# Kernel tuning notes

Hardware: AMD Instinct MI355X
Metric: run time of the kernel (lower is better)

Reference implementation:

```python
import jax, jax.numpy as jnp
import numpy as np

N_NODES = 50000
N_EDGES = 800000
NODE_DIM = 128
EDGE_DIM = 10
IN_DIM = 2 * NODE_DIM + EDGE_DIM
BN_EPS = 1e-5


def setup_inputs() -> dict:
    key = jax.random.key(0)
    ks = jax.random.split(key, 8)
    h = jax.random.normal(ks[0], (N_NODES, NODE_DIM), dtype=jnp.float32)
    edge_index = jax.random.randint(ks[1], (2, N_EDGES), 0, N_NODES, dtype=jnp.int64)
    edge_feat = jax.random.normal(ks[2], (N_EDGES, EDGE_DIM), dtype=jnp.float32)
    scale = 1.0 / np.sqrt(IN_DIM)
    gate_w = jax.random.normal(ks[3], (IN_DIM, NODE_DIM), dtype=jnp.float32) * scale
    gate_b = jax.random.normal(ks[4], (NODE_DIM,), dtype=jnp.float32) * scale
    cand_w = jax.random.normal(ks[5], (IN_DIM, NODE_DIM), dtype=jnp.float32) * scale
    cand_b = jax.random.normal(ks[6], (NODE_DIM,), dtype=jnp.float32) * scale
    bn_gamma = jnp.ones((NODE_DIM,), dtype=jnp.float32)
    bn_beta = jnp.zeros((NODE_DIM,), dtype=jnp.float32)
    return {"h": h, "edge_index": edge_index, "edge_feat": edge_feat,
            "gate_w": gate_w, "gate_b": gate_b, "cand_w": cand_w, "cand_b": cand_b,
            "bn_gamma": bn_gamma, "bn_beta": bn_beta}


def reference(h, edge_index, edge_feat, gate_w, gate_b, cand_w, cand_b, bn_gamma, bn_beta):
    src = edge_index[0]
    dst = edge_index[1]
    # gather endpoint features and concat with edge features: [E, 2*D + De]
    z = jnp.concatenate([h[src], h[dst], edge_feat], axis=1)
    g = jax.nn.sigmoid(z @ gate_w + gate_b)   # [E, D]
    c = jax.nn.softplus(z @ cand_w + cand_b)  # [E, D]
    m = g * c
    # scatter-add messages to source nodes (matches index_add_(0, src, m))
    agg = jax.ops.segment_sum(m, src, num_segments=h.shape[0])
    # BatchNorm1d in training mode: batch mean / biased variance over nodes
    mean = jnp.mean(agg, axis=0)
    var = jnp.var(agg, axis=0)
    agg_bn = (agg - mean) * jax.lax.rsqrt(var + BN_EPS) * bn_gamma + bn_beta
    return jax.nn.softplus(h + agg_bn)
```

## Files before the change

### kernel.cpp

```cpp
#include <hip/hip_runtime.h>
#include <math.h>

#define N_NODES 50000
#define N_EDGES 800000
#define D 128
#define DE 10
#define K_TOT 266
#define TE 64
#define N_TILES (N_EDGES / TE)
#define ZSTRIDE 296
#define MSTRIDE 129
#define WP_ELEMS (9 * 16 * 64 * 8)
#define SCAN_BLOCKS 196
#define CSTRIDE 16

typedef __bf16 bf16x8 __attribute__((ext_vector_type(8)));
typedef __bf16 bf16x4 __attribute__((ext_vector_type(4)));
typedef __bf16 bf16x2 __attribute__((ext_vector_type(2)));
typedef float  f32x4  __attribute__((ext_vector_type(4)));

__device__ __forceinline__ float fast_sigmoid(float x) {
    float t = __builtin_amdgcn_exp2f(-1.44269504089f * x);
    return __builtin_amdgcn_rcpf(1.0f + t);
}
__device__ __forceinline__ float fast_softplus(float x) {
    float t = __builtin_amdgcn_exp2f(-1.44269504089f * fabsf(x));
    return fmaxf(x, 0.0f) + 0.69314718056f * __builtin_amdgcn_logf(1.0f + t);
}

__global__ __launch_bounds__(256) void prep(
    const float* __restrict__ h, const float* __restrict__ gw,
    const float* __restrict__ cw, const int* __restrict__ ei,
    __bf16* __restrict__ hb, __bf16* __restrict__ wp,
    int* __restrict__ counts)
{
    int bx = blockIdx.x, t = threadIdx.x;
    if (bx < 6250) {
        int i4 = bx * 256 + t;
        float4 v = *(const float4*)&h[(size_t)i4 * 4];
        bf16x4 o = { (__bf16)v.x, (__bf16)v.y, (__bf16)v.z, (__bf16)v.w };
        *(bf16x4*)&hb[(size_t)i4 * 4] = o;
    } else if (bx < 6538) {
        int idx = (bx - 6250) * 256 + t;
        if (idx < WP_ELEMS) {
            int j    = idx & 7;
            int lane = (idx >> 3) & 63;
            int nb   = (idx >> 9) & 15;
            int kb   = idx >> 13;
            int k    = kb * 32 + ((lane >> 4) << 3) + j;
            int col  = ((nb >> 1) << 4) + (lane & 15);
            const float* w = (nb & 1) ? cw : gw;
            float v = (k < K_TOT) ? w[k * D + col] : 0.0f;
            wp[idx] = (__bf16)v;
        }
    } else {
        int e = (bx - 6538) * 256 + t;
        atomicAdd(&counts[ei[e] * CSTRIDE], 1);
    }
}

__global__ __launch_bounds__(256) void scan_partials(
    const int* __restrict__ counts, int* __restrict__ bsum)
{
    __shared__ int ss[256];
    int t = threadIdx.x;
    int i = blockIdx.x * 256 + t;
    int c = (i < N_NODES) ? counts[i * CSTRIDE] : 0;
    ss[t] = c;
    __syncthreads();
    #pragma unroll
    for (int off = 1; off < 256; off <<= 1) {
        int v = (t >= off) ? ss[t - off] : 0;
        __syncthreads();
        ss[t] += v;
        __syncthreads();
    }
    if (t == 255) bsum[blockIdx.x] = ss[255];
}

__global__ __launch_bounds__(256) void scan_final(
    int* __restrict__ counts, const int* __restrict__ bsum)
{
    __shared__ int sb[256];
    __shared__ int ss[256];
    int t = threadIdx.x;
    sb[t] = (t < SCAN_BLOCKS) ? bsum[t] : 0;
    int i = blockIdx.x * 256 + t;
    int c = (i < N_NODES) ? counts[i * CSTRIDE] : 0;
    ss[t] = c;
    __syncthreads();
    #pragma unroll
    for (int off = 1; off < 256; off <<= 1) {
        int v  = (t >= off) ? ss[t - off] : 0;
        int vb = (t >= off) ? sb[t - off] : 0;
        __syncthreads();
        ss[t] += v;
        sb[t] += vb;
        __syncthreads();
    }
    int base = blockIdx.x ? sb[blockIdx.x - 1] : 0;
    if (i < N_NODES) counts[i * CSTRIDE] = base + ss[t] - c;
}

__global__ __launch_bounds__(256) void csr_scatter(
    const int* __restrict__ ei, int* __restrict__ cursor,
    int2* __restrict__ sdp, int* __restrict__ eidx)
{
    int e = blockIdx.x * 256 + threadIdx.x;
    int node = ei[e];
    int pos = atomicAdd(&cursor[node * CSTRIDE], 1);
    sdp[pos] = make_int2(node, ei[N_EDGES + e]);
    eidx[pos] = e;
}

__global__ __launch_bounds__(256, 4) void edge_mfma_scatter(
    const __bf16* __restrict__ hb, const int2* __restrict__ sdp,
    const float* __restrict__ ef, const __bf16* __restrict__ wp,
    const float* __restrict__ gb, const float* __restrict__ cb,
    const int* __restrict__ eidx, float* __restrict__ agg)
{
    __shared__ __align__(16) unsigned char smem[TE * ZSTRIDE * 2];
    __shared__ int s_eid[TE], s_src[TE], s_dst[TE];
    __bf16* zs = (__bf16*)smem;
    float*  ms = (float*)smem;

    const int t  = threadIdx.x;
    const int e0 = blockIdx.x * TE;

    if (t < TE) {
        int2 p = sdp[e0 + t];
        s_src[t] = p.x;
        s_dst[t] = p.y;
        s_eid[t] = eidx[e0 + t];
    }
    __syncthreads();

    #pragma unroll
    for (int it = 0; it < 8; ++it) {
        int lin = it * 256 + t;
        int region = lin >> 10;
        int r   = (lin >> 4) & 63;
        int seg = lin & 15;
        int node = region ? s_dst[r] : s_src[r];
        bf16x8 v = *(const bf16x8*)&hb[(size_t)node * D + seg * 8];
        *(bf16x8*)&zs[r * ZSTRIDE + region * 128 + seg * 8] = v;
    }
    if (t < TE) {
        const float* efr = &ef[(size_t)s_eid[t] * DE];
        __bf16* row = &zs[t * ZSTRIDE + 256];
        #pragma unroll
        for (int j = 0; j < 5; ++j) {
            float2 a = *(const float2*)&efr[j * 2];
            bf16x2 p = { (__bf16)a.x, (__bf16)a.y };
            *(bf16x2*)&row[j * 2] = p;
        }
        *(bf16x2*)&row[10] = (bf16x2)(__bf16)0.0f;
        *(bf16x4*)&row[12] = (bf16x4)(__bf16)0.0f;
        *(bf16x8*)&row[16] = (bf16x8)(__bf16)0.0f;
        *(bf16x8*)&row[24] = (bf16x8)(__bf16)0.0f;
    }
    __syncthreads();

    const int w     = t >> 6;
    const int l     = t & 63;
    const int quad  = l >> 4;
    const int col16 = l & 15;

    f32x4 acc[4][4];
    #pragma unroll
    for (int mt = 0; mt < 4; ++mt)
        #pragma unroll
        for (int nt = 0; nt < 4; ++nt)
            acc[mt][nt] = (f32x4)0.0f;

    const __bf16* zp  = &zs[col16 * ZSTRIDE + quad * 8];
    const __bf16* wpp = &wp[(size_t)((w * 4) * 64 + l) * 8];

    #pragma unroll
    for (int kb = 0; kb < 9; ++kb) {
        bf16x8 afr[4];
        #pragma unroll
        for (int mt = 0; mt < 4; ++mt)
            afr[mt] = *(const bf16x8*)&zp[mt * 16 * ZSTRIDE + kb * 32];
        bf16x8 bfr[4];
        #pragma unroll
        for (int nt = 0; nt < 4; ++nt)
            bfr[nt] = *(const bf16x8*)&wpp[(size_t)(kb * 16 + nt) * 512];
        #pragma unroll
        for (int mt = 0; mt < 4; ++mt)
            #pragma unroll
            for (int nt = 0; nt < 4; ++nt)
                acc[mt][nt] = __builtin_amdgcn_mfma_f32_16x16x32_bf16(
                    afr[mt], bfr[nt], acc[mt][nt], 0, 0, 0);
    }
    __syncthreads();

    const int colA = w * 32 + col16;
    const int colB = colA + 16;
    const float gbA = gb[colA], cbA = cb[colA];
    const float gbB = gb[colB], cbB = cb[colB];

    #pragma unroll
    for (int mt = 0; mt < 4; ++mt) {
        #pragma unroll
        for (int r = 0; r < 4; ++r) {
            int e = mt * 16 + quad * 4 + r;
            ms[e * MSTRIDE + colA] =
                fast_sigmoid(acc[mt][0][r] + gbA) * fast_softplus(acc[mt][1][r] + cbA);
            ms[e * MSTRIDE + colB] =
                fast_sigmoid(acc[mt][2][r] + gbB) * fast_softplus(acc[mt][3][r] + cbB);
        }
    }
    __syncthreads();

    const int half = t >> 7;
    const int c    = t & 127;
    const int rlo  = half * 32, rhi = rlo + 32;
    int   cur = s_src[rlo];
    float s   = 0.0f;
    for (int e = rlo; e < rhi; ++e) {
        int node = s_src[e];
        float v  = ms[e * MSTRIDE + c];
        if (node != cur) {
            atomicAdd(&agg[(size_t)cur * D + c], s);
            s = 0.0f; cur = node;
        }
        s += v;
    }
    atomicAdd(&agg[(size_t)cur * D + c], s);
}

__global__ __launch_bounds__(256) void col_stats(
    const float* __restrict__ agg, float* __restrict__ stats)
{
    const int t    = threadIdx.x;
    const int col  = t & 127;
    const int half = t >> 7;
    float s = 0.0f, s2 = 0.0f;
    for (int r = blockIdx.x * 2 + half; r < N_NODES; r += gridDim.x * 2) {
        float v = agg[(size_t)r * D + col];
        s += v; s2 += v * v;
    }
    atomicAdd(&stats[col], s);
    atomicAdd(&stats[128 + col], s2);
}

__global__ __launch_bounds__(256) void out_softplus(
    const float* __restrict__ h, const float* __restrict__ agg,
    const float* __restrict__ stats, const float* __restrict__ gamma,
    const float* __restrict__ beta, float* __restrict__ out)
{
    __shared__ float sc[128], bi[128];
    int t = threadIdx.x;
    if (t < 128) {
        const float inv_n = 1.0f / (float)N_NODES;
        float mean = stats[t] * inv_n;
        float var  = stats[128 + t] * inv_n - mean * mean;
        var = fmaxf(var, 0.0f);
        float rstd = rsqrtf(var + 1e-5f);
        float s = rstd * gamma[t];
        sc[t] = s;
        bi[t] = beta[t] - mean * s;
    }
    __syncthreads();
    int idx4 = blockIdx.x * 256 + t;
    int base = idx4 * 4;
    if (base < N_NODES * D) {
        float4 hv = *(const float4*)&h[base];
        float4 av = *(const float4*)&agg[base];
        int c = base & 127;
        float4 o;
        o.x = fast_softplus(hv.x + av.x * sc[c + 0] + bi[c + 0]);
        o.y = fast_softplus(hv.y + av.y * sc[c + 1] + bi[c + 1]);
        o.z = fast_softplus(hv.z + av.z * sc[c + 2] + bi[c + 2]);
        o.w = fast_softplus(hv.w + av.w * sc[c + 3] + bi[c + 3]);
        *(float4*)&out[base] = o;
    }
}

extern "C" void kernel_launch(void* const* d_in, const int* in_sizes, int n_in,
                              void* d_out, int out_size, void* d_ws, size_t ws_size,
                              hipStream_t stream) {
    const float* h     = (const float*)d_in[0];
    const int*   ei    = (const int*)  d_in[1];
    const float* ef    = (const float*)d_in[2];
    const float* gw    = (const float*)d_in[3];
    const float* gb    = (const float*)d_in[4];
    const float* cw    = (const float*)d_in[5];
    const float* cb    = (const float*)d_in[6];
    const float* gamma = (const float*)d_in[7];
    const float* beta  = (const float*)d_in[8];
    float* out = (float*)d_out;

    float*  agg     = (float*)d_ws;
    float*  stats   = agg + (size_t)N_NODES * D;
    int*    counts  = (int*)(stats + 256);
    int*    bsum    = counts + N_NODES * CSTRIDE;
    __bf16* wp      = (__bf16*)(bsum + 256);
    __bf16* hb      = wp + WP_ELEMS;
    int2*   sdp     = (int2*)(hb + (size_t)N_NODES * D);
    int*    eidx    = (int*)(sdp + N_EDGES);

    const size_t zero_bytes = ((size_t)N_NODES * D + 256) * sizeof(float)
                            + (size_t)N_NODES * CSTRIDE * sizeof(int);
    hipMemsetAsync(d_ws, 0, zero_bytes, stream);
    prep<<<9663, 256, 0, stream>>>(h, gw, cw, ei, hb, wp, counts);
    scan_partials<<<SCAN_BLOCKS, 256, 0, stream>>>(counts, bsum);
    scan_final<<<SCAN_BLOCKS, 256, 0, stream>>>(counts, bsum);
    csr_scatter<<<N_EDGES / 256, 256, 0, stream>>>(ei, counts, sdp, eidx);
    edge_mfma_scatter<<<N_TILES, 256, 0, stream>>>(hb, sdp, ef, wp, gb, cb, eidx, agg);
    col_stats<<<784, 256, 0, stream>>>(agg, stats);
    out_softplus<<<(N_NODES * D / 4 + 255) / 256, 256, 0, stream>>>(
        h, agg, stats, gamma, beta, out);
}
```

Baseline: 414.2 us.

## Merge preprocessing and finishing kernels into cooperative grid-synced kernels

Replaces the memset, prep, two scan kernels and CSR scatter with one cooperative kernel that uses grid-wide syncs between phases. It also merges column stats and the output softplus into a second cooperative kernel. Column sums are pre-reduced in shared memory before the atomics. The aim is to cut launch and inter-kernel gaps. The cost is grid.sync overhead and a fixed grid of 1024 blocks doing grid-stride loops.

```diff
diff --git a/kernel.cpp b/kernel.cpp
--- a/kernel.cpp
+++ b/kernel.cpp
@@ -1,5 +1,8 @@
 #include <hip/hip_runtime.h>
+#include <hip/hip_cooperative_groups.h>
 #include <math.h>
+
+namespace cg = cooperative_groups;
 
 #define N_NODES 50000
 #define N_EDGES 800000
@@ -13,6 +16,8 @@
 #define WP_ELEMS (9 * 16 * 64 * 8)
 #define SCAN_BLOCKS 196
 #define CSTRIDE 16
+#define CB_GRID 1024
+#define CF_GRID 1024
 
 typedef __bf16 bf16x8 __attribute__((ext_vector_type(8)));
 typedef __bf16 bf16x4 __attribute__((ext_vector_type(4)));
@@ -28,89 +33,89 @@
     return fmaxf(x, 0.0f) + 0.69314718056f * __builtin_amdgcn_logf(1.0f + t);
 }
 
-__global__ __launch_bounds__(256) void prep(
+__global__ __launch_bounds__(256) void coop_build(
     const float* __restrict__ h, const float* __restrict__ gw,
     const float* __restrict__ cw, const int* __restrict__ ei,
     __bf16* __restrict__ hb, __bf16* __restrict__ wp,
-    int* __restrict__ counts)
+    int* __restrict__ counts, int* __restrict__ bsum,
+    int2* __restrict__ sdp, int* __restrict__ eidx,
+    float* __restrict__ agg, float* __restrict__ stats)
 {
-    int bx = blockIdx.x, t = threadIdx.x;
-    if (bx < 6250) {
-        int i4 = bx * 256 + t;
-        float4 v = *(const float4*)&h[(size_t)i4 * 4];
+    cg::grid_group grid = cg::this_grid();
+    __shared__ int ss[256];
+    __shared__ int sb[256];
+    const int t    = threadIdx.x;
+    const int gtid = blockIdx.x * 256 + t;
+    const int nthr = CB_GRID * 256;
+
+    for (int i = gtid; i < N_NODES * D / 4; i += nthr) {
+        *(float4*)&agg[(size_t)i * 4] = make_float4(0.f, 0.f, 0.f, 0.f);
+        float4 v = *(const float4*)&h[(size_t)i * 4];
         bf16x4 o = { (__bf16)v.x, (__bf16)v.y, (__bf16)v.z, (__bf16)v.w };
-        *(bf16x4*)&hb[(size_t)i4 * 4] = o;
-    } else if (bx < 6538) {
-        int idx = (bx - 6250) * 256 + t;
-        if (idx < WP_ELEMS) {
-            int j    = idx & 7;
-            int lane = (idx >> 3) & 63;
-            int nb   = (idx >> 9) & 15;
-            int kb   = idx >> 13;
-            int k    = kb * 32 + ((lane >> 4) << 3) + j;
-            int col  = ((nb >> 1) << 4) + (lane & 15);
-            const float* w = (nb & 1) ? cw : gw;
-            float v = (k < K_TOT) ? w[k * D + col] : 0.0f;
-            wp[idx] = (__bf16)v;
-        }
-    } else {
-        int e = (bx - 6538) * 256 + t;
+        *(bf16x4*)&hb[(size_t)i * 4] = o;
+    }
+    if (gtid < 256) stats[gtid] = 0.0f;
+    for (int i = gtid; i < N_NODES * CSTRIDE / 4; i += nthr)
+        *(int4*)&counts[(size_t)i * 4] = make_int4(0, 0, 0, 0);
+    for (int idx = gtid; idx < WP_ELEMS; idx += nthr) {
+        int j    = idx & 7;
+        int lane = (idx >> 3) & 63;
+        int nb   = (idx >> 9) & 15;
+        int kb   = idx >> 13;
+        int k    = kb * 32 + ((lane >> 4) << 3) + j;
+        int col  = ((nb >> 1) << 4) + (lane & 15);
+        const float* w = (nb & 1) ? cw : gw;
+        float v = (k < K_TOT) ? w[k * D + col] : 0.0f;
+        wp[idx] = (__bf16)v;
+    }
+    grid.sync();
+
+    for (int e = gtid; e < N_EDGES; e += nthr)
         atomicAdd(&counts[ei[e] * CSTRIDE], 1);
-    }
-}
-
-__global__ __launch_bounds__(256) void scan_partials(
-    const int* __restrict__ counts, int* __restrict__ bsum)
-{
-    __shared__ int ss[256];
-    int t = threadIdx.x;
-    int i = blockIdx.x * 256 + t;
-    int c = (i < N_NODES) ? counts[i * CSTRIDE] : 0;
-    ss[t] = c;
-    __syncthreads();
-    #pragma unroll
-    for (int off = 1; off < 256; off <<= 1) {
-        int v = (t >= off) ? ss[t - off] : 0;
+    grid.sync();
+
+    if (blockIdx.x < SCAN_BLOCKS) {
+        int i = blockIdx.x * 256 + t;
+        int c = (i < N_NODES) ? counts[i * CSTRIDE] : 0;
+        ss[t] = c;
         __syncthreads();
-        ss[t] += v;
+        #pragma unroll
+        for (int off = 1; off < 256; off <<= 1) {
+            int v = (t >= off) ? ss[t - off] : 0;
+            __syncthreads();
+            ss[t] += v;
+            __syncthreads();
+        }
+        if (t == 255) bsum[blockIdx.x] = ss[255];
+    }
+    grid.sync();
+
+    if (blockIdx.x < SCAN_BLOCKS) {
+        sb[t] = (t < SCAN_BLOCKS) ? bsum[t] : 0;
+        int i = blockIdx.x * 256 + t;
+        int c = (i < N_NODES) ? counts[i * CSTRIDE] : 0;
+        ss[t] = c;
         __syncthreads();
-    }
-    if (t == 255) bsum[blockIdx.x] = ss[255];
-}
-
-__global__ __launch_bounds__(256) void scan_final(
-    int* __restrict__ counts, const int* __restrict__ bsum)
-{
-    __shared__ int sb[256];
-    __shared__ int ss[256];
-    int t = threadIdx.x;
-    sb[t] = (t < SCAN_BLOCKS) ? bsum[t] : 0;
-    int i = blockIdx.x * 256 + t;
-    int c = (i < N_NODES) ? counts[i * CSTRIDE] : 0;
-    ss[t] = c;
-    __syncthreads();
-    #pragma unroll
-    for (int off = 1; off < 256; off <<= 1) {
-        int v  = (t >= off) ? ss[t - off] : 0;
-        int vb = (t >= off) ? sb[t - off] : 0;
-        __syncthreads();
-        ss[t] += v;
-        sb[t] += vb;
-        __syncthreads();
-    }
-    int base = blockIdx.x ? sb[blockIdx.x - 1] : 0;
-    if (i < N_NODES) counts[i * CSTRIDE] = base + ss[t] - c;
-}
-
-__global__ __launch_bounds__(256) void csr_scatter(
-    const int* __restrict__ ei, int* __restrict__ cursor,
-    int2* __restrict__ sdp, int* __restrict__ eidx)
-{
-    int e = blockIdx.x * 256 + threadIdx.x;
-    int node = ei[e];
-    int pos = atomicAdd(&cursor[node * CSTRIDE], 1);
-    sdp[pos] = make_int2(node, ei[N_EDGES + e]);
-    eidx[pos] = e;
+        #pragma unroll
+        for (int off = 1; off < 256; off <<= 1) {
+            int v  = (t >= off) ? ss[t - off] : 0;
+            int vb = (t >= off) ? sb[t - off] : 0;
+            __syncthreads();
+            ss[t] += v;
+            sb[t] += vb;
+            __syncthreads();
+        }
+        int base = blockIdx.x ? sb[blockIdx.x - 1] : 0;
+        if (i < N_NODES) counts[i * CSTRIDE] = base + ss[t] - c;
+    }
+    grid.sync();
+
+    for (int e = gtid; e < N_EDGES; e += nthr) {
+        int node = ei[e];
+        int pos = atomicAdd(&counts[node * CSTRIDE], 1);
+        sdp[pos] = make_int2(node, ei[N_EDGES + e]);
+        eidx[pos] = e;
+    }
 }
 
 __global__ __launch_bounds__(256, 4) void edge_mfma_scatter(
@@ -230,42 +235,46 @@
     atomicAdd(&agg[(size_t)cur * D + c], s);
 }
 
-__global__ __launch_bounds__(256) void col_stats(
-    const float* __restrict__ agg, float* __restrict__ stats)
+__global__ __launch_bounds__(256) void coop_finish(
+    const float* __restrict__ h, const float* __restrict__ agg,
+    const float* __restrict__ gamma, const float* __restrict__ beta,
+    float* __restrict__ stats, float* __restrict__ out)
 {
+    cg::grid_group grid = cg::this_grid();
+    __shared__ float red[256];
+    __shared__ float sc[128], bi[128];
     const int t    = threadIdx.x;
     const int col  = t & 127;
     const int half = t >> 7;
+
     float s = 0.0f, s2 = 0.0f;
-    for (int r = blockIdx.x * 2 + half; r < N_NODES; r += gridDim.x * 2) {
+    for (int r = blockIdx.x * 2 + half; r < N_NODES; r += CF_GRID * 2) {
         float v = agg[(size_t)r * D + col];
         s += v; s2 += v * v;
     }
-    atomicAdd(&stats[col], s);
-    atomicAdd(&stats[128 + col], s2);
-}
-
-__global__ __launch_bounds__(256) void out_softplus(
-    const float* __restrict__ h, const float* __restrict__ agg,
-    const float* __restrict__ stats, const float* __restrict__ gamma,
-    const float* __restrict__ beta, float* __restrict__ out)
-{
-    __shared__ float sc[128], bi[128];
-    int t = threadIdx.x;
+    red[t] = s;
+    __syncthreads();
+    if (half == 0) atomicAdd(&stats[col], s + red[128 + col]);
+    __syncthreads();
+    red[t] = s2;
+    __syncthreads();
+    if (half == 0) atomicAdd(&stats[128 + col], s2 + red[128 + col]);
+    grid.sync();
+
     if (t < 128) {
         const float inv_n = 1.0f / (float)N_NODES;
         float mean = stats[t] * inv_n;
         float var  = stats[128 + t] * inv_n - mean * mean;
         var = fmaxf(var, 0.0f);
         float rstd = rsqrtf(var + 1e-5f);
-        float s = rstd * gamma[t];
-        sc[t] = s;
-        bi[t] = beta[t] - mean * s;
-    }
-    __syncthreads();
-    int idx4 = blockIdx.x * 256 + t;
-    int base = idx4 * 4;
-    if (base < N_NODES * D) {
+        float g = rstd * gamma[t];
+        sc[t] = g;
+        bi[t] = beta[t] - mean * g;
+    }
+    __syncthreads();
+    const int gtid = blockIdx.x * 256 + t;
+    for (int i4 = gtid; i4 < N_NODES * D / 4; i4 += CF_GRID * 256) {
+        int base = i4 * 4;
         float4 hv = *(const float4*)&h[base];
         float4 av = *(const float4*)&agg[base];
         int c = base & 127;
@@ -301,15 +310,16 @@
     int2*   sdp     = (int2*)(hb + (size_t)N_NODES * D);
     int*    eidx    = (int*)(sdp + N_EDGES);
 
-    const size_t zero_bytes = ((size_t)N_NODES * D + 256) * sizeof(float)
-                            + (size_t)N_NODES * CSTRIDE * sizeof(int);
-    hipMemsetAsync(d_ws, 0, zero_bytes, stream);
-    prep<<<9663, 256, 0, stream>>>(h, gw, cw, ei, hb, wp, counts);
-    scan_partials<<<SCAN_BLOCKS, 256, 0, stream>>>(counts, bsum);
-    scan_final<<<SCAN_BLOCKS, 256, 0, stream>>>(counts, bsum);
-    csr_scatter<<<N_EDGES / 256, 256, 0, stream>>>(ei, counts, sdp, eidx);
+    void* argsB[] = { (void*)&h, (void*)&gw, (void*)&cw, (void*)&ei,
+                      (void*)&hb, (void*)&wp, (void*)&counts, (void*)&bsum,
+                      (void*)&sdp, (void*)&eidx, (void*)&agg, (void*)&stats };
+    hipLaunchCooperativeKernel((const void*)coop_build, dim3(CB_GRID), dim3(256),
+                               argsB, 0, stream);
+
     edge_mfma_scatter<<<N_TILES, 256, 0, stream>>>(hb, sdp, ef, wp, gb, cb, eidx, agg);
-    col_stats<<<784, 256, 0, stream>>>(agg, stats);
-    out_softplus<<<(N_NODES * D / 4 + 255) / 256, 256, 0, stream>>>(
-        h, agg, stats, gamma, beta, out);
-}
+
+    void* argsF[] = { (void*)&h, (void*)&agg, (void*)&gamma, (void*)&beta,
+                      (void*)&stats, (void*)&out };
+    hipLaunchCooperativeKernel((const void*)coop_finish, dim3(CF_GRID), dim3(256),
+                               argsF, 0, stream);
+}
```

Result: slower. 894.8 us (+116.0%).
